# Performance work log

Measured on AMD Instinct MI355X. Metric: run time of the kernel, lower is better.

## Reference

```python
import jax, jax.numpy as jnp
import numpy as np

B, N, C, Q, H, RATIO = 8, 8700, 256, 300, 8, 4
D = C // H
HID = C * RATIO
EPS = 1e-5


def _ln(x, w, b):
    m = jnp.mean(x, axis=-1, keepdims=True)
    v = jnp.mean((x - m) ** 2, axis=-1, keepdims=True)
    return (x - m) * jax.lax.rsqrt(v + EPS) * w + b


def setup_inputs() -> dict:
    key = jax.random.key(0)
    ks = jax.random.split(key, 8)
    s = 0.02
    return {
        "x": jax.random.normal(ks[0], (B, N, C), jnp.float32),
        # linear weights stored [in, out] (y = x @ W), no biases (qkv_bias=False, Mlp bias=False)
        "Wq": jax.random.normal(ks[1], (C, C), jnp.float32) * s,
        "Wk": jax.random.normal(ks[2], (C, C), jnp.float32) * s,
        "Wv": jax.random.normal(ks[3], (C, C), jnp.float32) * s,
        "Wp": jax.random.normal(ks[4], (C, C), jnp.float32) * s,
        "W1": jax.random.normal(ks[5], (C, HID), jnp.float32) * s,
        "W2": jax.random.normal(ks[6], (HID, C), jnp.float32) * s,
        "ln1_w": jnp.ones((C,), jnp.float32),
        "ln1_b": jnp.zeros((C,), jnp.float32),
        "ln2_w": jnp.ones((C,), jnp.float32),
        "ln2_b": jnp.zeros((C,), jnp.float32),
        "gamma1": jnp.ones((C,), jnp.float32),
        "gamma2": jnp.ones((C,), jnp.float32),
    }


def reference(x, Wq, Wk, Wv, Wp, W1, W2, ln1_w, ln1_b, ln2_w, ln2_b, gamma1, gamma2):
    scale = D ** -0.5
    xn = _ln(x, ln1_w, ln1_b)                       # [B,N,C]
    # SAQAttn: queries only from the first Q tokens; keys/values from all N tokens
    q = (xn[:, :Q] @ Wq).reshape(B, Q, H, D) * scale  # [B,Q,H,D]
    k = (xn @ Wk).reshape(B, N, H, D)
    v = (xn @ Wv).reshape(B, N, H, D)
    attn = jax.nn.softmax(jnp.einsum('bqhd,bnhd->bhqn', q, k), axis=-1)  # [B,H,Q,N]
    x_det = jnp.einsum('bhqn,bnhd->bqhd', attn, v).reshape(B, Q, C) @ Wp  # [B,Q,C]
    # residual with layer-scale gamma1; context tokens pass normed features through
    x_attn = jnp.concatenate([x_det, xn[:, Q:]], axis=1)
    x = x + gamma1 * x_attn
    # tokens_norm=False: norm2 only on query tokens
    x = jnp.concatenate([_ln(x[:, :Q], ln2_w, ln2_b), x[:, Q:]], axis=1)
    # MLP on query tokens with layer-scale gamma2 (exact GELU, as nn.GELU default)
    det = gamma2 * (jax.nn.gelu(x[:, :Q] @ W1, approximate=False) @ W2)
    # faithful to source: x_res + cat([det, x[:,Q:]]) doubles the context tokens
    return x + jnp.concatenate([det, x[:, Q:]], axis=1)
```

## Files before the change

### kernel.cpp

```cpp
#include <hip/hip_runtime.h>

#define BB 8
#define NN 8700
#define CC 256
#define QQ 300
#define HH 8
#define DD 32
#define HIDN 1024
#define NSPLIT 16
#define TSTR (NSPLIT * 64)
#define KSLACK 1536

typedef unsigned short u16;
typedef __attribute__((ext_vector_type(8))) short short8;
typedef __attribute__((ext_vector_type(4))) float f32x4;

#define MFMA16(a, b, c) __builtin_amdgcn_mfma_f32_16x16x32_bf16((a), (b), (c), 0, 0, 0)

__device__ __forceinline__ unsigned int cvtpk(float lo, float hi) {
    unsigned int r;
    asm("v_cvt_pk_bf16_f32 %0, %1, %2" : "=v"(r) : "v"(lo), "v"(hi));
    return r;
}
__device__ __forceinline__ u16 f2b_hw(float f) { return (u16)cvtpk(f, 0.f); }
__device__ __forceinline__ float b2f(u16 u) {
    unsigned int x = ((unsigned int)u) << 16;
    return __builtin_bit_cast(float, x);
}
__device__ __forceinline__ void gload16(const u16* g, u16* l) {
    __builtin_amdgcn_global_load_lds(
        (const __attribute__((address_space(1))) void*)g,
        (__attribute__((address_space(3))) void*)l, 16, 0, 0);
}

__global__ __launch_bounds__(256)
void prep_k(const float* __restrict__ x, const float* __restrict__ ln1w,
            const float* __restrict__ ln1b, const float* __restrict__ g1,
            u16* __restrict__ xn, float* __restrict__ out,
            const float* __restrict__ Wq, const float* __restrict__ Wk,
            const float* __restrict__ Wv, const float* __restrict__ Wp,
            const float* __restrict__ W1, const float* __restrict__ W2,
            u16* __restrict__ wdst, float qscale)
{
    __shared__ u16 tl[64][66];
    if (blockIdx.x < 17400) {
        int row = blockIdx.x * 4 + (threadIdx.x >> 6);
        int l = threadIdx.x & 63;
        size_t base = (size_t)row * CC + l * 4;
        float4 xv = *reinterpret_cast<const float4*>(x + base);
        float s  = xv.x + xv.y + xv.z + xv.w;
        float s2 = xv.x * xv.x + xv.y * xv.y + xv.z * xv.z + xv.w * xv.w;
#pragma unroll
        for (int m = 1; m < 64; m <<= 1) {
            s  += __shfl_xor(s,  m, 64);
            s2 += __shfl_xor(s2, m, 64);
        }
        float mean = s * (1.0f / CC);
        float rs = rsqrtf(s2 * (1.0f / CC) - mean * mean + 1e-5f);
        float4 wv = *reinterpret_cast<const float4*>(ln1w + l * 4);
        float4 bb = *reinterpret_cast<const float4*>(ln1b + l * 4);
        float n0 = (xv.x - mean) * rs * wv.x + bb.x;
        float n1 = (xv.y - mean) * rs * wv.y + bb.y;
        float n2 = (xv.z - mean) * rs * wv.z + bb.z;
        float n3 = (xv.w - mean) * rs * wv.w + bb.w;
        uint2 u; u.x = cvtpk(n0, n1); u.y = cvtpk(n2, n3);
        *reinterpret_cast<uint2*>(xn + base) = u;
        int n = row % NN;
        if (n >= QQ) {
            float4 gv = *reinterpret_cast<const float4*>(g1 + l * 4);
            float4 o;
            o.x = 2.0f * (xv.x + gv.x * n0);
            o.y = 2.0f * (xv.y + gv.y * n1);
            o.z = 2.0f * (xv.z + gv.z * n2);
            o.w = 2.0f * (xv.w + gv.w * n3);
            *reinterpret_cast<float4*>(out + base) = o;
        }
    } else {
        int bid = blockIdx.x - 17400;
        const float* src; int K, N, tr, tc; size_t dof; float sc = 1.f;
        if (bid < 64) {
            int mat = bid >> 4, ti = bid & 15;
            src = (mat == 0) ? Wq : (mat == 1) ? Wk : (mat == 2) ? Wv : Wp;
            K = 256; N = 256; tr = ti >> 2; tc = ti & 3;
            dof = (size_t)mat * 65536;
            if (mat == 0) sc = qscale;
        } else if (bid < 128) {
            int ti = bid - 64; src = W1; K = 256; N = 1024; tr = ti >> 4; tc = ti & 15; dof = 262144;
        } else {
            int ti = bid - 128; src = W2; K = 1024; N = 256; tr = ti >> 2; tc = ti & 3; dof = 524288;
        }
        int tid = threadIdx.x;
        int jj = tid & 63;
        int i0 = tid >> 6;
#pragma unroll
        for (int ii = 0; ii < 16; ii++) {
            int kk = i0 * 16 + ii;
            float v = src[(size_t)(tr * 64 + kk) * N + tc * 64 + jj] * sc;
            tl[kk][jj] = f2b_hw(v);
        }
        __syncthreads();
#pragma unroll
        for (int ii = 0; ii < 16; ii++) {
            int nn = i0 * 16 + ii;
            wdst[dof + (size_t)(tc * 64 + nn) * K + tr * 64 + jj] = tl[jj][nn];
        }
    }
}

__global__ __launch_bounds__(512)
void gemm_kv(const u16* __restrict__ A, const u16* __restrict__ WT,
             u16* __restrict__ Cb, u16* __restrict__ Cb2, int M)
{
    __shared__ u16 alds[64 * 256];
    const int tid = threadIdx.x;
    const int w = tid >> 6, l = tid & 63;
    const int l15 = l & 15, kg = l >> 4;
    const int rowbase = blockIdx.x * 64;
    const f32x4 fz = {0.f, 0.f, 0.f, 0.f};

    {
        const char* gb = (const char*)(A + (size_t)rowbase * CC);
        char* lb = (char*)alds;
#pragma unroll
        for (int j = 0; j < 4; j++) {
            int o = tid * 64 + j * 16;
            short8 v = *reinterpret_cast<const short8*>(gb + o);
            int d = o ^ (((o >> 9) & 7) << 4);
            *reinterpret_cast<short8*>(lb + d) = v;
        }
    }
    __syncthreads();

    const int colbase = w * 64;
    const u16* bp[4];
#pragma unroll
    for (int ni = 0; ni < 4; ni++)
        bp[ni] = WT + (size_t)(colbase + ni * 16 + l15) * CC + kg * 8;

    f32x4 acc[4][4];
#pragma unroll
    for (int mi = 0; mi < 4; mi++)
#pragma unroll
        for (int ni = 0; ni < 4; ni++) acc[mi][ni] = fz;

    const char* lb = (const char*)alds;
    const int sw = (l15 & 7) << 4;
    int abase[4];
#pragma unroll
    for (int mi = 0; mi < 4; mi++) abase[mi] = (mi * 16 + l15) << 9;

#pragma unroll
    for (int ks = 0; ks < 8; ks++) {
        const int koff = ((ks * 64) + (kg * 16)) ^ sw;
        short8 a[4], bfr[4];
#pragma unroll
        for (int mi = 0; mi < 4; mi++)
            a[mi] = *reinterpret_cast<const short8*>(lb + abase[mi] + koff);
#pragma unroll
        for (int ni = 0; ni < 4; ni++)
            bfr[ni] = *reinterpret_cast<const short8*>(bp[ni] + ks * 32);
#pragma unroll
        for (int mi = 0; mi < 4; mi++)
#pragma unroll
            for (int ni = 0; ni < 4; ni++)
                acc[mi][ni] = MFMA16(bfr[ni], a[mi], acc[mi][ni]);
    }

#pragma unroll
    for (int mi = 0; mi < 4; mi++) {
        int r = rowbase + mi * 16 + l15;
        if (r >= M) continue;
#pragma unroll
        for (int ni = 0; ni < 4; ni++) {
            int col0 = colbase + ni * 16 + kg * 4;
            f32x4 v = acc[mi][ni];
            uint2 pk; pk.x = cvtpk(v[0], v[1]); pk.y = cvtpk(v[2], v[3]);
            if (col0 < CC) *reinterpret_cast<uint2*>(Cb  + (size_t)r * CC + col0)        = pk;
            else           *reinterpret_cast<uint2*>(Cb2 + (size_t)r * CC + (col0 - CC)) = pk;
        }
    }
}

__global__ __launch_bounds__(256)
void gemm_q(const u16* __restrict__ A, const u16* __restrict__ WT, u16* __restrict__ Cb, int M)
{
    const int w = threadIdx.x >> 6, l = threadIdx.x & 63;
    const int l15 = l & 15, kg = l >> 4;
    const int rowbase = blockIdx.x * 16;
    const int colbase = w * 64;
    const short8 z8 = {0, 0, 0, 0, 0, 0, 0, 0};
    const f32x4 fz = {0.f, 0.f, 0.f, 0.f};

    int r = rowbase + l15;
    bool av = (r < M);
    int rr = av ? r : 0;
    const u16* ap = A + ((size_t)(rr / QQ) * NN + (rr % QQ)) * CC + kg * 8;
    const u16* bp[4];
#pragma unroll
    for (int ni = 0; ni < 4; ni++)
        bp[ni] = WT + (size_t)(colbase + ni * 16 + l15) * CC + kg * 8;

    f32x4 acc[4];
#pragma unroll
    for (int ni = 0; ni < 4; ni++) acc[ni] = fz;

    for (int ks = 0; ks < CC; ks += 32) {
        short8 a = av ? *reinterpret_cast<const short8*>(ap + ks) : z8;
#pragma unroll
        for (int ni = 0; ni < 4; ni++) {
            short8 bfr = *reinterpret_cast<const short8*>(bp[ni] + ks);
            acc[ni] = MFMA16(bfr, a, acc[ni]);
        }
    }
    if (r < M) {
#pragma unroll
        for (int ni = 0; ni < 4; ni++) {
            int col0 = colbase + ni * 16 + kg * 4;
            uint2 pk; pk.x = cvtpk(acc[ni][0], acc[ni][1]); pk.y = cvtpk(acc[ni][2], acc[ni][3]);
            *reinterpret_cast<uint2*>(Cb + (size_t)r * CC + col0) = pk;
        }
    }
}

__global__ __launch_bounds__(256)
void attn_k(const u16* __restrict__ qm, const u16* __restrict__ km,
            const u16* __restrict__ vm, u16* __restrict__ Opb,
            float* __restrict__ lp)
{
    __shared__ u16 klds[2][64 * 32];
    __shared__ u16 vt[2][32 * 64];
    __shared__ u16 plds[4][2][16 * 64];

    const int bx = blockIdx.x;
    const int split = bx >> 6;
    const int rem = bx & 63;
    const int h = rem >> 3, b = rem & 7;
    const int bh = b * HH + h;
    const int tid = threadIdx.x;
    const int w = tid >> 6, l = tid & 63;
    const int l15 = l & 15, kg = l >> 4;
    const int tstart = split * 64;
    const int nt = (NN - tstart + TSTR - 1) / TSTR;

    const f32x4 fz = {0.f, 0.f, 0.f, 0.f};
    const short os = (short)0x3F80;
    const short8 ones = {os, os, os, os, os, os, os, os};

    const u16* kbase = km + (size_t)b * NN * CC + h * DD;
    const u16* vbase = vm + (size_t)b * NN * CC + h * DD;
    const int vkp = (tid & 31) * 2;
    const int vdg = (tid >> 5) * 4;

    const int krow  = (w << 4) + (l >> 2);
    const int kslot = (l & 3) ^ ((krow >> 1) & 3);
    const u16* ksrc = kbase + (size_t)krow * CC + kslot * 8;

    short8 qfr[5];
#pragma unroll
    for (int qf = 0; qf < 5; qf++) {
        int qrow = w * 80 + qf * 16 + l15;
        int qc = qrow < QQ ? qrow : 0;
        qfr[qf] = *reinterpret_cast<const short8*>(qm + ((size_t)(b * QQ + qc) * CC + h * DD + kg * 8));
    }

    f32x4 o[2][5]; float lpart[5];
#pragma unroll
    for (int qf = 0; qf < 5; qf++) { o[0][qf] = fz; o[1][qf] = fz; lpart[qf] = 0.f; }

    gload16(ksrc + (size_t)tstart * CC, (u16*)((char*)klds[0] + (w << 10)));
    ushort4 v0r = *reinterpret_cast<const ushort4*>(vbase + (size_t)(tstart + vkp) * CC + vdg);
    ushort4 v1r = *reinterpret_cast<const ushort4*>(vbase + (size_t)(tstart + vkp + 1) * CC + vdg);

    char* pl = (char*)plds[w];
    const int rdswz = ((l15 << 7) ^ ((l15 & 7) << 4)) + (kg << 4);
    const int wrbase = (l15 << 7) ^ ((l15 & 7) << 4);

    for (int t = 0; t < nt; ++t) {
        const int n0 = tstart + t * TSTR;
        char* vtb = (char*)vt[t & 1];
#pragma unroll
        for (int i = 0; i < 4; i++) {
            int row = vdg + i;
            unsigned int pk2 = (unsigned int)v0r[i] | ((unsigned int)v1r[i] << 16);
            int byteo = ((row << 7) + (vkp << 1)) ^ ((row & 7) << 4);
            *reinterpret_cast<unsigned int*>(vtb + byteo) = pk2;
        }
        __syncthreads();

        gload16(ksrc + (size_t)(n0 + TSTR) * CC, (u16*)((char*)klds[(t + 1) & 1] + (w << 10)));
        ushort4 v0n = *reinterpret_cast<const ushort4*>(vbase + (size_t)(n0 + TSTR + vkp) * CC + vdg);
        ushort4 v1n = *reinterpret_cast<const ushort4*>(vbase + (size_t)(n0 + TSTR + vkp + 1) * CC + vdg);

        short8 kf[4];
        { const char* klb = (const char*)klds[t & 1];
#pragma unroll
          for (int kb = 0; kb < 4; kb++) {
              int row = kb * 16 + l15;
              int off = (row << 6) + ((kg ^ ((row >> 1) & 3)) << 4);
              kf[kb] = *reinterpret_cast<const short8*>(klb + off);
          } }

        short8 va[2][2];
#pragma unroll
        for (int ks = 0; ks < 2; ks++)
#pragma unroll
            for (int dg = 0; dg < 2; dg++) {
                int row = dg * 16 + l15;
                int byteo = ((row << 7) + 64 * ks + 16 * kg) ^ ((row & 7) << 4);
                va[ks][dg] = *reinterpret_cast<const short8*>(vtb + byteo);
            }

        const bool tail = (n0 + 64 > NN);

#pragma unroll
        for (int qf = 0; qf < 5; qf++) {
            short8 bp0, bp1;
            if (qf > 0) {
                const char* plr = pl + (((qf - 1) & 1) << 11);
                bp0 = *reinterpret_cast<const short8*>(plr + rdswz);
                bp1 = *reinterpret_cast<const short8*>(plr + rdswz + 64);
            }
            f32x4 s[4];
            __builtin_amdgcn_s_setprio(1);
#pragma unroll
            for (int kb = 0; kb < 4; kb++)
                s[kb] = MFMA16(kf[kb], qfr[qf], fz);
            __builtin_amdgcn_s_setprio(0);
            char* plw = pl + ((qf & 1) << 11);
#pragma unroll
            for (int kb = 0; kb < 4; kb++) {
                float p0 = exp2f(s[kb][0]);
                float p1 = exp2f(s[kb][1]);
                float p2 = exp2f(s[kb][2]);
                float p3 = exp2f(s[kb][3]);
                if (tail) {
                    int kbase2 = n0 + 16 * kb + 4 * kg;
                    if (kbase2 + 0 >= NN) p0 = 0.f;
                    if (kbase2 + 1 >= NN) p1 = 0.f;
                    if (kbase2 + 2 >= NN) p2 = 0.f;
                    if (kbase2 + 3 >= NN) p3 = 0.f;
                }
                uint2 pw; pw.x = cvtpk(p0, p1); pw.y = cvtpk(p2, p3);
                *reinterpret_cast<uint2*>(plw + (wrbase + ((16 * kb + 4 * kg) << 1))) = pw;
            }
            if (qf > 0) {
                __builtin_amdgcn_s_setprio(1);
                o[0][qf - 1] = MFMA16(va[0][0], bp0, o[0][qf - 1]);
                o[1][qf - 1] = MFMA16(va[0][1], bp0, o[1][qf - 1]);
                o[0][qf - 1] = MFMA16(va[1][0], bp1, o[0][qf - 1]);
                o[1][qf - 1] = MFMA16(va[1][1], bp1, o[1][qf - 1]);
                f32x4 tsum = MFMA16(ones, bp0, fz);
                tsum = MFMA16(ones, bp1, tsum);
                __builtin_amdgcn_s_setprio(0);
                lpart[qf - 1] += tsum[0];
            }
        }
        {
            const char* plr = pl + 0;
            short8 bp0 = *reinterpret_cast<const short8*>(plr + rdswz);
            short8 bp1 = *reinterpret_cast<const short8*>(plr + rdswz + 64);
            __builtin_amdgcn_s_setprio(1);
            o[0][4] = MFMA16(va[0][0], bp0, o[0][4]);
            o[1][4] = MFMA16(va[0][1], bp0, o[1][4]);
            o[0][4] = MFMA16(va[1][0], bp1, o[0][4]);
            o[1][4] = MFMA16(va[1][1], bp1, o[1][4]);
            f32x4 tsum = MFMA16(ones, bp0, fz);
            tsum = MFMA16(ones, bp1, tsum);
            __builtin_amdgcn_s_setprio(0);
            lpart[4] += tsum[0];
        }
        v0r = v0n; v1r = v1n;
    }

    size_t pb = (size_t)(split * 64 + bh) * QQ;
#pragma unroll
    for (int qf = 0; qf < 5; qf++) {
        int q = w * 80 + qf * 16 + l15;
        if (q >= QQ) continue;
        size_t pr = pb + q;
        if (kg == 0) lp[pr] = lpart[qf];
        uint2 w0; w0.x = cvtpk(o[0][qf][0], o[0][qf][1]); w0.y = cvtpk(o[0][qf][2], o[0][qf][3]);
        uint2 w1; w1.x = cvtpk(o[1][qf][0], o[1][qf][1]); w1.y = cvtpk(o[1][qf][2], o[1][qf][3]);
        *reinterpret_cast<uint2*>(Opb + pr * DD + kg * 4)      = w0;
        *reinterpret_cast<uint2*>(Opb + pr * DD + 16 + kg * 4) = w1;
    }
}

__global__ __launch_bounds__(256)
void cpl_k(const u16* __restrict__ Opb, const float* __restrict__ lp,
           const u16* __restrict__ WpT, const float* __restrict__ x,
           const float* __restrict__ g1, const float* __restrict__ w2,
           const float* __restrict__ b2, float* __restrict__ xqf, u16* __restrict__ xqb)
{
    __shared__ u16 albs[16 * 256];
    __shared__ float pdl[16][260];

    const int tid = threadIdx.x;
    const int r0 = blockIdx.x * 16;

    {
        int row = tid >> 4, cg = tid & 15;
        int r = r0 + row;
        int b = r / QQ, q = r - b * QQ;
        int h = cg >> 1;
        int dbase = (cg & 1) * 16;
        float acc[16];
#pragma unroll
        for (int j = 0; j < 16; j++) acc[j] = 0.f;
        float L = 0.f;
        for (int s = 0; s < NSPLIT; s++) {
            size_t pr = ((size_t)(s * 64) + b * 8 + h) * QQ + q;
            L += lp[pr];
            short8 v0 = *reinterpret_cast<const short8*>(Opb + pr * DD + dbase);
            short8 v1 = *reinterpret_cast<const short8*>(Opb + pr * DD + dbase + 8);
#pragma unroll
            for (int j = 0; j < 8; j++) {
                acc[j]     += b2f((u16)v0[j]);
                acc[8 + j] += b2f((u16)v1[j]);
            }
        }
        float inv = 1.0f / L;
        short8 o0, o1;
#pragma unroll
        for (int j = 0; j < 4; j++) {
            unsigned int a = cvtpk(acc[2 * j] * inv, acc[2 * j + 1] * inv);
            unsigned int bq = cvtpk(acc[8 + 2 * j] * inv, acc[9 + 2 * j] * inv);
            o0[2 * j] = (short)(a & 0xffff); o0[2 * j + 1] = (short)(a >> 16);
            o1[2 * j] = (short)(bq & 0xffff); o1[2 * j + 1] = (short)(bq >> 16);
        }
        char* lb = (char*)albs;
        int byte0 = (row << 9) + (cg << 5);
        *reinterpret_cast<short8*>(lb + ((byte0)      ^ ((row & 7) << 4))) = o0;
        *reinterpret_cast<short8*>(lb + ((byte0 + 16) ^ ((row & 7) << 4))) = o1;
    }
    __syncthreads();

    const int w = tid >> 6, l = tid & 63;
    const int l15 = l & 15, kg = l >> 4;
    {
        const f32x4 fz = {0.f, 0.f, 0.f, 0.f};
        const int colbase = w * 64;
        const u16* bp[4];
#pragma unroll
        for (int ni = 0; ni < 4; ni++)
            bp[ni] = WpT + (size_t)(colbase + ni * 16 + l15) * CC + kg * 8;
        f32x4 acc[4];
#pragma unroll
        for (int ni = 0; ni < 4; ni++) acc[ni] = fz;
        const char* lb = (const char*)albs;
        const int arow = l15 << 9;
        const int sw = (l15 & 7) << 4;
#pragma unroll
        for (int ks = 0; ks < 8; ks++) {
            short8 a = *reinterpret_cast<const short8*>(lb + (arow + ((kg * 16 + ks * 64) ^ sw)));
#pragma unroll
            for (int ni = 0; ni < 4; ni++) {
                short8 bfr = *reinterpret_cast<const short8*>(bp[ni] + ks * 32);
                acc[ni] = MFMA16(bfr, a, acc[ni]);
            }
        }
#pragma unroll
        for (int ni = 0; ni < 4; ni++) {
            float4 v; v.x = acc[ni][0]; v.y = acc[ni][1]; v.z = acc[ni][2]; v.w = acc[ni][3];
            *reinterpret_cast<float4*>(&pdl[l15][colbase + ni * 16 + kg * 4]) = v;
        }
    }
    __syncthreads();

    {
        int row = tid >> 4, cg = tid & 15;
        int r = r0 + row;
        int b = r / QQ, q = r - b * QQ;
        size_t xoff = ((size_t)b * NN + q) * CC + cg * 16;
        float val[16];
        float s = 0.f, s2 = 0.f;
#pragma unroll
        for (int j4 = 0; j4 < 4; j4++) {
            float4 xv = *reinterpret_cast<const float4*>(x + xoff + j4 * 4);
            float4 gv = *reinterpret_cast<const float4*>(g1 + cg * 16 + j4 * 4);
            int c = cg * 16 + j4 * 4;
            val[j4 * 4 + 0] = xv.x + gv.x * pdl[row][c + 0];
            val[j4 * 4 + 1] = xv.y + gv.y * pdl[row][c + 1];
            val[j4 * 4 + 2] = xv.z + gv.z * pdl[row][c + 2];
            val[j4 * 4 + 3] = xv.w + gv.w * pdl[row][c + 3];
#pragma unroll
            for (int j = 0; j < 4; j++) {
                float v = val[j4 * 4 + j];
                s += v; s2 += v * v;
            }
        }
#pragma unroll
        for (int m = 1; m < 16; m <<= 1) {
            s  += __shfl_xor(s,  m, 64);
            s2 += __shfl_xor(s2, m, 64);
        }
        float mean = s * (1.0f / CC);
        float rs = rsqrtf(s2 * (1.0f / CC) - mean * mean + 1e-5f);
        size_t roff = (size_t)r * CC + cg * 16;
#pragma unroll
        for (int j4 = 0; j4 < 4; j4++) {
            int c = cg * 16 + j4 * 4;
            float4 wv = *reinterpret_cast<const float4*>(w2 + c);
            float4 bb = *reinterpret_cast<const float4*>(b2 + c);
            float n0 = (val[j4 * 4 + 0] - mean) * rs * wv.x + bb.x;
            float n1 = (val[j4 * 4 + 1] - mean) * rs * wv.y + bb.y;
            float n2 = (val[j4 * 4 + 2] - mean) * rs * wv.z + bb.z;
            float n3 = (val[j4 * 4 + 3] - mean) * rs * wv.w + bb.w;
            float4 o; o.x = n0; o.y = n1; o.z = n2; o.w = n3;
            *reinterpret_cast<float4*>(xqf + roff + j4 * 4) = o;
            uint2 u; u.x = cvtpk(n0, n1); u.y = cvtpk(n2, n3);
            *reinterpret_cast<uint2*>(xqb + roff + j4 * 4) = u;
        }
    }
}

__global__ __launch_bounds__(256)
void mlp_k(const u16* __restrict__ xqb, const u16* __restrict__ W1T,
           const u16* __restrict__ W2T, const float* __restrict__ xqf,
           const float* __restrict__ g2, float* __restrict__ out)
{
    __shared__ u16 h1l[16 * 1024];

    const int tid = threadIdx.x;
    const int w = tid >> 6, l = tid & 63;
    const int l15 = l & 15, kg = l >> 4;
    const int r0 = blockIdx.x * 16;
    const f32x4 fz = {0.f, 0.f, 0.f, 0.f};

    {
        const u16* ap = xqb + (size_t)(r0 + l15) * CC + kg * 8;
        f32x4 acc[16];
#pragma unroll
        for (int ni = 0; ni < 16; ni++) acc[ni] = fz;
#pragma unroll
        for (int ks = 0; ks < 8; ks++) {
            short8 a = *reinterpret_cast<const short8*>(ap + ks * 32);
#pragma unroll
            for (int ni = 0; ni < 16; ni++) {
                const u16* bp = W1T + (size_t)(w * 256 + ni * 16 + l15) * CC + kg * 8 + ks * 32;
                short8 bfr = *reinterpret_cast<const short8*>(bp);
                acc[ni] = MFMA16(bfr, a, acc[ni]);
            }
        }
        char* lb = (char*)h1l;
        const int sw = (l15 & 7) << 4;
#pragma unroll
        for (int ni = 0; ni < 16; ni++) {
            float g0 = 0.5f * acc[ni][0] * (1.0f + erff(acc[ni][0] * 0.70710678118654752f));
            float g1v = 0.5f * acc[ni][1] * (1.0f + erff(acc[ni][1] * 0.70710678118654752f));
            float g2v = 0.5f * acc[ni][2] * (1.0f + erff(acc[ni][2] * 0.70710678118654752f));
            float g3 = 0.5f * acc[ni][3] * (1.0f + erff(acc[ni][3] * 0.70710678118654752f));
            uint2 pk; pk.x = cvtpk(g0, g1v); pk.y = cvtpk(g2v, g3);
            int byteo = (l15 << 11) + (((w * 256 + ni * 16 + kg * 4) << 1) ^ sw);
            *reinterpret_cast<uint2*>(lb + byteo) = pk;
        }
    }
    __syncthreads();

    {
        const int colbase = w * 64;
        const u16* bp[4];
#pragma unroll
        for (int ni = 0; ni < 4; ni++)
            bp[ni] = W2T + (size_t)(colbase + ni * 16 + l15) * HIDN + kg * 8;
        f32x4 acc[4];
#pragma unroll
        for (int ni = 0; ni < 4; ni++) acc[ni] = fz;
        const char* lb = (const char*)h1l;
        const int arow = l15 << 11;
        const int sw = (l15 & 7) << 4;
#pragma unroll
        for (int ks = 0; ks < 32; ks++) {
            short8 a = *reinterpret_cast<const short8*>(lb + arow + (((kg * 8 + ks * 32) << 1) ^ sw));
#pragma unroll
            for (int ni = 0; ni < 4; ni++) {
                short8 bfr = *reinterpret_cast<const short8*>(bp[ni] + ks * 32);
                acc[ni] = MFMA16(bfr, a, acc[ni]);
            }
        }
        int r = r0 + l15;
        size_t orow = (size_t)(r / QQ) * NN + (r % QQ);
#pragma unroll
        for (int ni = 0; ni < 4; ni++) {
            int col0 = colbase + ni * 16 + kg * 4;
            float4 xv = *reinterpret_cast<const float4*>(xqf + (size_t)r * CC + col0);
            float4 gv = *reinterpret_cast<const float4*>(g2 + col0);
            float4 o;
            o.x = xv.x + gv.x * acc[ni][0];
            o.y = xv.y + gv.y * acc[ni][1];
            o.z = xv.z + gv.z * acc[ni][2];
            o.w = xv.w + gv.w * acc[ni][3];
            *reinterpret_cast<float4*>(out + orow * CC + col0) = o;
        }
    }
}

extern "C" void kernel_launch(void* const* d_in, const int* in_sizes, int n_in,
                              void* d_out, int out_size, void* d_ws, size_t ws_size,
                              hipStream_t stream)
{
    (void)in_sizes; (void)n_in; (void)out_size; (void)ws_size;
    const float* x    = (const float*)d_in[0];
    const float* Wq   = (const float*)d_in[1];
    const float* Wk   = (const float*)d_in[2];
    const float* Wv   = (const float*)d_in[3];
    const float* Wp   = (const float*)d_in[4];
    const float* W1   = (const float*)d_in[5];
    const float* W2   = (const float*)d_in[6];
    const float* ln1w = (const float*)d_in[7];
    const float* ln1b = (const float*)d_in[8];
    const float* ln2w = (const float*)d_in[9];
    const float* ln2b = (const float*)d_in[10];
    const float* g1   = (const float*)d_in[11];
    const float* g2   = (const float*)d_in[12];
    float* out = (float*)d_out;

    char* p = (char*)d_ws;
    auto alloc = [&](size_t bytes) { char* r = p; p += (bytes + 255) & ~(size_t)255; return r; };

    const size_t MKV = (size_t)BB * NN;
    const size_t MQ  = (size_t)BB * QQ;

    u16* WqT  = (u16*)alloc((size_t)CC * CC * 2);
    u16* WkvT = (u16*)alloc((size_t)CC * CC * 2 * 2);
    u16* WpT  = (u16*)alloc((size_t)CC * CC * 2);
    u16* W1T  = (u16*)alloc((size_t)CC * HIDN * 2);
    u16* W2T  = (u16*)alloc((size_t)HIDN * CC * 2);
    u16* xn   = (u16*)alloc((MKV + 64) * CC * 2);
    u16* kbf  = (u16*)alloc((MKV + KSLACK) * CC * 2);
    u16* vbf  = (u16*)alloc((MKV + KSLACK) * CC * 2);
    u16* qbf  = (u16*)alloc(MQ * CC * 2);
    u16* xqb  = (u16*)alloc(MQ * CC * 2);
    float* xqf = (float*)alloc(MQ * CC * 4);
    u16* Opb  = (u16*)alloc((size_t)NSPLIT * 64 * QQ * DD * 2);
    float* lp  = (float*)alloc((size_t)NSPLIT * 64 * QQ * 4);

    const float qscale = 0.17677669529663687f * 1.4426950408889634f;

    prep_k<<<17592, 256, 0, stream>>>(x, ln1w, ln1b, g1, xn, out,
                                      Wq, Wk, Wv, Wp, W1, W2, WqT, qscale);

    gemm_kv<<<1088, 512, 0, stream>>>(xn, WkvT, kbf, vbf, (int)MKV);
    gemm_q<<<150, 256, 0, stream>>>(xn, WqT, qbf, (int)MQ);

    attn_k<<<64 * NSPLIT, 256, 0, stream>>>(qbf, kbf, vbf, Opb, lp);

    cpl_k<<<150, 256, 0, stream>>>(Opb, lp, WpT, x, g1, ln2w, ln2b, xqf, xqb);

    mlp_k<<<150, 256, 0, stream>>>(xqb, W1T, W2T, xqf, g2, out);
}
```

Measured before the change: 225.2 us.

## Store Q/K/V in head-major contiguous layout for attention streaming

The KV and Q projection GEMMs now write their outputs as [head][batch][token][32] with padded token stride, instead of token-major rows of 256 channels. The attention kernel then reads each head's K/V as contiguous 64-byte rows, so its global loads touch dense memory rather than 64-byte strided slices of 512-byte rows. The cost moves to the GEMM epilogue, which now issues scattered 8-byte stores and does a per-row integer division.

```diff
diff --git a/kernel.cpp b/kernel.cpp
--- a/kernel.cpp
+++ b/kernel.cpp
@@ -10,6 +10,7 @@
 #define NSPLIT 16
 #define TSTR (NSPLIT * 64)
 #define KSLACK 1536
+#define PADN (NN + KSLACK)
 
 typedef unsigned short u16;
 typedef __attribute__((ext_vector_type(8))) short short8;
@@ -170,13 +171,17 @@
     for (int mi = 0; mi < 4; mi++) {
         int r = rowbase + mi * 16 + l15;
         if (r >= M) continue;
+        int bb = r / NN, n = r - bb * NN;
 #pragma unroll
         for (int ni = 0; ni < 4; ni++) {
             int col0 = colbase + ni * 16 + kg * 4;
             f32x4 v = acc[mi][ni];
             uint2 pk; pk.x = cvtpk(v[0], v[1]); pk.y = cvtpk(v[2], v[3]);
-            if (col0 < CC) *reinterpret_cast<uint2*>(Cb  + (size_t)r * CC + col0)        = pk;
-            else           *reinterpret_cast<uint2*>(Cb2 + (size_t)r * CC + (col0 - CC)) = pk;
+            int c = (col0 < CC) ? col0 : col0 - CC;
+            int hb = (c >> 5) * BB + bb;
+            size_t off = ((size_t)hb * PADN + n) * DD + (c & 31);
+            if (col0 < CC) *reinterpret_cast<uint2*>(Cb  + off) = pk;
+            else           *reinterpret_cast<uint2*>(Cb2 + off) = pk;
         }
     }
 }
@@ -213,11 +218,13 @@
         }
     }
     if (r < M) {
+        int bb = r / QQ, q = r - bb * QQ;
 #pragma unroll
         for (int ni = 0; ni < 4; ni++) {
             int col0 = colbase + ni * 16 + kg * 4;
             uint2 pk; pk.x = cvtpk(acc[ni][0], acc[ni][1]); pk.y = cvtpk(acc[ni][2], acc[ni][3]);
-            *reinterpret_cast<uint2*>(Cb + (size_t)r * CC + col0) = pk;
+            int hb = (col0 >> 5) * BB + bb;
+            *reinterpret_cast<uint2*>(Cb + ((size_t)hb * QQ + q) * DD + (col0 & 31)) = pk;
         }
     }
 }
@@ -236,6 +243,7 @@
     const int rem = bx & 63;
     const int h = rem >> 3, b = rem & 7;
     const int bh = b * HH + h;
+    const int hb = h * BB + b;
     const int tid = threadIdx.x;
     const int w = tid >> 6, l = tid & 63;
     const int l15 = l & 15, kg = l >> 4;
@@ -246,30 +254,31 @@
     const short os = (short)0x3F80;
     const short8 ones = {os, os, os, os, os, os, os, os};
 
-    const u16* kbase = km + (size_t)b * NN * CC + h * DD;
-    const u16* vbase = vm + (size_t)b * NN * CC + h * DD;
+    const u16* kbase = km + (size_t)hb * PADN * DD;
+    const u16* vbase = vm + (size_t)hb * PADN * DD;
+    const u16* qbase = qm + (size_t)hb * QQ * DD;
     const int vkp = (tid & 31) * 2;
     const int vdg = (tid >> 5) * 4;
 
     const int krow  = (w << 4) + (l >> 2);
     const int kslot = (l & 3) ^ ((krow >> 1) & 3);
-    const u16* ksrc = kbase + (size_t)krow * CC + kslot * 8;
+    const u16* ksrc = kbase + krow * DD + kslot * 8;
 
     short8 qfr[5];
 #pragma unroll
     for (int qf = 0; qf < 5; qf++) {
         int qrow = w * 80 + qf * 16 + l15;
         int qc = qrow < QQ ? qrow : 0;
-        qfr[qf] = *reinterpret_cast<const short8*>(qm + ((size_t)(b * QQ + qc) * CC + h * DD + kg * 8));
+        qfr[qf] = *reinterpret_cast<const short8*>(qbase + (size_t)qc * DD + kg * 8);
     }
 
     f32x4 o[2][5]; float lpart[5];
 #pragma unroll
     for (int qf = 0; qf < 5; qf++) { o[0][qf] = fz; o[1][qf] = fz; lpart[qf] = 0.f; }
 
-    gload16(ksrc + (size_t)tstart * CC, (u16*)((char*)klds[0] + (w << 10)));
-    ushort4 v0r = *reinterpret_cast<const ushort4*>(vbase + (size_t)(tstart + vkp) * CC + vdg);
-    ushort4 v1r = *reinterpret_cast<const ushort4*>(vbase + (size_t)(tstart + vkp + 1) * CC + vdg);
+    gload16(ksrc + (size_t)tstart * DD, (u16*)((char*)klds[0] + (w << 10)));
+    ushort4 v0r = *reinterpret_cast<const ushort4*>(vbase + (size_t)(tstart + vkp) * DD + vdg);
+    ushort4 v1r = *reinterpret_cast<const ushort4*>(vbase + (size_t)(tstart + vkp + 1) * DD + vdg);
 
     char* pl = (char*)plds[w];
     const int rdswz = ((l15 << 7) ^ ((l15 & 7) << 4)) + (kg << 4);
@@ -287,9 +296,9 @@
         }
         __syncthreads();
 
-        gload16(ksrc + (size_t)(n0 + TSTR) * CC, (u16*)((char*)klds[(t + 1) & 1] + (w << 10)));
-        ushort4 v0n = *reinterpret_cast<const ushort4*>(vbase + (size_t)(n0 + TSTR + vkp) * CC + vdg);
-        ushort4 v1n = *reinterpret_cast<const ushort4*>(vbase + (size_t)(n0 + TSTR + vkp + 1) * CC + vdg);
+        gload16(ksrc + (size_t)(n0 + TSTR) * DD, (u16*)((char*)klds[(t + 1) & 1] + (w << 10)));
+        ushort4 v0n = *reinterpret_cast<const ushort4*>(vbase + (size_t)(n0 + TSTR + vkp) * DD + vdg);
+        ushort4 v1n = *reinterpret_cast<const ushort4*>(vbase + (size_t)(n0 + TSTR + vkp + 1) * DD + vdg);
 
         short8 kf[4];
         { const char* klb = (const char*)klds[t & 1];
@@ -627,9 +636,9 @@
     u16* W1T  = (u16*)alloc((size_t)CC * HIDN * 2);
     u16* W2T  = (u16*)alloc((size_t)HIDN * CC * 2);
     u16* xn   = (u16*)alloc((MKV + 64) * CC * 2);
-    u16* kbf  = (u16*)alloc((MKV + KSLACK) * CC * 2);
-    u16* vbf  = (u16*)alloc((MKV + KSLACK) * CC * 2);
-    u16* qbf  = (u16*)alloc(MQ * CC * 2);
+    u16* kbf  = (u16*)alloc((size_t)64 * PADN * DD * 2);
+    u16* vbf  = (u16*)alloc((size_t)64 * PADN * DD * 2);
+    u16* qbf  = (u16*)alloc((size_t)64 * QQ * DD * 2);
     u16* xqb  = (u16*)alloc(MQ * CC * 2);
     float* xqf = (float*)alloc(MQ * CC * 4);
     u16* Opb  = (u16*)alloc((size_t)NSPLIT * 64 * QQ * DD * 2);
```

Result: faster. 219.4 us (-2.6%).
